# Optimization experiments

Hardware: AMD Instinct MI355X
Metric: run time of the kernel (lower is better)

## Reference

```python
import jax, jax.numpy as jnp
import numpy as np

B, T_ENC, T_DEC, D, N_STATE = 32, 1024, 512, 512, 512


def setup_inputs() -> dict:
    key = jax.random.key(0)
    k1, k2, k3, k4 = jax.random.split(key, 4)
    scale = 1.0 / np.sqrt(D)
    return {
        "states_encoder": jax.random.normal(k1, (B, T_ENC, D), dtype=jnp.float32),
        "states_decoder": jax.random.normal(k2, (B, T_DEC, N_STATE), dtype=jnp.float32),
        "Wk": jax.random.normal(k3, (D, N_STATE), dtype=jnp.float32) * scale,
        "bk": jnp.zeros((N_STATE,), dtype=jnp.float32),
        "Wv": jax.random.normal(k4, (D, N_STATE), dtype=jnp.float32) * scale,
        "bv": jnp.zeros((N_STATE,), dtype=jnp.float32),
    }


def reference(states_encoder, states_decoder, Wk, bk, Wv, bv):
    # general Luong dot-product attention (n_state = int branch)
    key_vector = states_encoder @ Wk + bk          # [B, T_enc, N]
    val_vector = states_encoder @ Wv + bv          # [B, T_enc, N]
    # score[b, t_dec, t_enc] = sum_n dec[b,t_dec,n] * key[b,t_enc,n]
    score = jnp.einsum('bqn,bkn->bqk', states_decoder, key_vector)
    attention = jax.nn.softmax(score, axis=-1)     # over encoder positions
    # context[b, t_dec, n] = sum_k attention[b,t_dec,k] * val[b,k,n]
    context = jnp.einsum('bqk,bkn->bqn', attention, val_vector)
    return (context, attention)
```

## Files before the change

### kernel.cpp

```cpp
#include <hip/hip_runtime.h>
#include <math.h>

#define BB    32
#define TENC  1024
#define TDEC  512
#define DDIM  512
#define NST   512

typedef _Float16 f16_t;
typedef _Float16 f16x8 __attribute__((ext_vector_type(8)));
typedef _Float16 f16x4 __attribute__((ext_vector_type(4)));
typedef float    f32x4 __attribute__((ext_vector_type(4)));

#define GLOAD_LDS16(gp, lp) __builtin_amdgcn_global_load_lds( \
    (const __attribute__((address_space(1))) unsigned int*)(const void*)(gp), \
    (__attribute__((address_space(3))) unsigned int*)(lp), 16, 0, 0)

static __device__ __forceinline__ f32x4 MFMA16H(f16x8 a, f16x8 b, f32x4 c) {
    return __builtin_amdgcn_mfma_f32_16x16x32_f16(a, b, c, 0, 0, 0);
}

__global__ __launch_bounds__(256)
void cvt_f32_f16(const float* __restrict__ x, f16_t* __restrict__ y, long n8)
{
    long i = (long)blockIdx.x * 256 + threadIdx.x;
    if (i >= n8) return;
    float4 a = *(const float4*)&x[i * 8];
    float4 b = *(const float4*)&x[i * 8 + 4];
    f16x8 o;
    o[0] = (f16_t)a.x; o[1] = (f16_t)a.y; o[2] = (f16_t)a.z; o[3] = (f16_t)a.w;
    o[4] = (f16_t)b.x; o[5] = (f16_t)b.y; o[6] = (f16_t)b.z; o[7] = (f16_t)b.w;
    *(f16x8*)&y[i * 8] = o;
}

__global__ __launch_bounds__(256)
void transpose_to_f16(const float* __restrict__ in, f16_t* __restrict__ out,
                      int R, int C)
{
    __shared__ f16_t tile[64][65];
    const int c0 = blockIdx.x * 64, r0 = blockIdx.y * 64;
    const int t = threadIdx.x;
    const int rr = t >> 4;
    const int cc = (t & 15) * 4;
#pragma unroll
    for (int p = 0; p < 4; ++p) {
        int r = rr + p * 16;
        float4 v = *(const float4*)&in[(long)(r0 + r) * C + c0 + cc];
        tile[r][cc + 0] = (f16_t)v.x;
        tile[r][cc + 1] = (f16_t)v.y;
        tile[r][cc + 2] = (f16_t)v.z;
        tile[r][cc + 3] = (f16_t)v.w;
    }
    __syncthreads();
    const int dr = t >> 2;
    const int tc = (t & 3) * 16;
    f16_t tmp[16];
#pragma unroll
    for (int e = 0; e < 16; ++e) tmp[e] = tile[tc + e][dr];
    *(f16x8*)&out[(long)(c0 + dr) * R + r0 + tc]     = *(f16x8*)&tmp[0];
    *(f16x8*)&out[(long)(c0 + dr) * R + r0 + tc + 8] = *(f16x8*)&tmp[8];
}

template<int EPI>
__global__ __launch_bounds__(256)
void gemm_h(const f16_t* __restrict__ A, const f16_t* __restrict__ B,
            const float* __restrict__ bias, void* __restrict__ C0,
            int M, int N, int K, long sA, long sB, long sC)
{
    __shared__ f16_t lds[2][8192];

    const int tid  = threadIdx.x;
    const int wave = tid >> 6;
    const int lane = tid & 63;

    const int gx = gridDim.x, gy = gridDim.y;
    const long nwg = (long)gx * gy * gridDim.z;
    const long fo  = ((long)blockIdx.z * gy + blockIdx.y) * gx + blockIdx.x;
    const long f2 = (fo & 7) * (nwg >> 3) + (fo >> 3);
    const int bx  = (int)(f2 % gx);
    const int by  = (int)((f2 / gx) % gy);
    const long bz = f2 / ((long)gx * gy);

    const f16_t* Ab = A + bz * sA;
    const f16_t* Bb = B + bz * sB;

    const int row0 = by * 128;
    const int col0 = bx * 128;

    const int srow  = wave * 16 + (lane >> 2);
    const int sslot = (lane & 3) ^ ((srow >> 1) & 3);
    const int wdst  = wave * 512;
    const long aOff0 = (long)(row0 + srow) * K + sslot * 8;
    const long aOff1 = (long)(row0 + 64 + srow) * K + sslot * 8;
    const long bOff0 = (long)(col0 + srow) * K + sslot * 8;
    const long bOff1 = (long)(col0 + 64 + srow) * K + sslot * 8;

    const int fr = lane & 15;
    const int q  = lane >> 4;
    const int wr = (wave >> 1) * 64;
    const int wc = (wave & 1) * 64;
    int aro[4], bro[4];
#pragma unroll
    for (int i = 0; i < 4; ++i) {
        const int r = wr + i * 16 + fr;
        aro[i] = r * 32 + ((q ^ ((r >> 1) & 3)) * 8);
    }
#pragma unroll
    for (int j = 0; j < 4; ++j) {
        const int r = wc + j * 16 + fr;
        bro[j] = r * 32 + ((q ^ ((r >> 1) & 3)) * 8);
    }

    f32x4 acc[4][4] = {};
    const int NT = K >> 5;

#define STAGE(buf, kt) do {                                   \
        GLOAD_LDS16(Ab + aOff0 + (kt), &(buf)[wdst]);         \
        GLOAD_LDS16(Ab + aOff1 + (kt), &(buf)[2048 + wdst]);  \
        GLOAD_LDS16(Bb + bOff0 + (kt), &(buf)[4096 + wdst]);  \
        GLOAD_LDS16(Bb + bOff1 + (kt), &(buf)[6144 + wdst]);  \
    } while (0)

    STAGE(lds[0], 0);

    for (int t = 0; t < NT; ++t) {
        const f16_t* cur = lds[t & 1];
        f16_t* nxt = lds[(t & 1) ^ 1];
        const bool pf = (t + 1 < NT);

        __builtin_amdgcn_sched_barrier(0);
        __builtin_amdgcn_s_barrier();
        if (pf) {
            STAGE(nxt, (t + 1) << 5);
            asm volatile("s_waitcnt vmcnt(4)" ::: "memory");
        } else {
            asm volatile("s_waitcnt vmcnt(0)" ::: "memory");
        }
        __builtin_amdgcn_s_barrier();
        __builtin_amdgcn_sched_barrier(0);

        f16x8 aH[4], bH[4];
#pragma unroll
        for (int i = 0; i < 4; ++i) aH[i] = *(const f16x8*)&cur[aro[i]];
#pragma unroll
        for (int j = 0; j < 4; ++j) bH[j] = *(const f16x8*)&cur[4096 + bro[j]];

#pragma unroll
        for (int j = 0; j < 4; ++j)
#pragma unroll
            for (int i = 0; i < 4; ++i)
                acc[i][j] = MFMA16H(aH[i], bH[j], acc[i][j]);
    }
#undef STAGE

    const int frow = q * 4;
#pragma unroll
    for (int i = 0; i < 4; ++i) {
        const int rgl = row0 + wr + i * 16 + frow;
#pragma unroll
        for (int j = 0; j < 4; ++j) {
            const int cg = col0 + wc + j * 16 + fr;
            if constexpr (EPI == 0) {
                float* C = (float*)C0 + bz * sC;
#pragma unroll
                for (int r = 0; r < 4; ++r)
                    C[(long)(rgl + r) * N + cg] = acc[i][j][r];
            } else if constexpr (EPI == 2) {
                f16_t* C = (f16_t*)C0 + bz * sC;
#pragma unroll
                for (int r = 0; r < 4; ++r)
                    C[(long)(rgl + r) * N + cg] = (f16_t)acc[i][j][r];
            } else {
                float* C = (float*)C0 + bz * sC;
                const float badd = bias[cg];
#pragma unroll
                for (int r = 0; r < 4; ++r)
                    C[(long)(rgl + r) * N + cg] = acc[i][j][r] + badd;
            }
        }
    }
}

__global__ __launch_bounds__(256)
void softmax_rows(float* __restrict__ S, f16_t* __restrict__ Sh)
{
    const long row = (long)blockIdx.x * 4 + (threadIdx.x >> 6);
    const int lane = threadIdx.x & 63;
    float* p = S + row * (long)TENC;

    float4 v[4];
    float m = -INFINITY;
#pragma unroll
    for (int i = 0; i < 4; ++i) {
        v[i] = *(const float4*)&p[i * 256 + lane * 4];
        m = fmaxf(fmaxf(fmaxf(v[i].x, v[i].y), fmaxf(v[i].z, v[i].w)), m);
    }
#pragma unroll
    for (int o = 32; o; o >>= 1) m = fmaxf(m, __shfl_xor(m, o, 64));

    float s = 0.f;
#pragma unroll
    for (int i = 0; i < 4; ++i) {
        v[i].x = __expf(v[i].x - m);
        v[i].y = __expf(v[i].y - m);
        v[i].z = __expf(v[i].z - m);
        v[i].w = __expf(v[i].w - m);
        s += v[i].x + v[i].y + v[i].z + v[i].w;
    }
#pragma unroll
    for (int o = 32; o; o >>= 1) s += __shfl_xor(s, o, 64);

    const float inv = 1.0f / s;
#pragma unroll
    for (int i = 0; i < 4; ++i) {
        v[i].x *= inv; v[i].y *= inv; v[i].z *= inv; v[i].w *= inv;
        *(float4*)&p[i * 256 + lane * 4] = v[i];
        if (Sh) {
            f16x4 h;
            h[0] = (f16_t)v[i].x; h[1] = (f16_t)v[i].y;
            h[2] = (f16_t)v[i].z; h[3] = (f16_t)v[i].w;
            *(f16x4*)&Sh[row * (long)TENC + i * 256 + lane * 4] = h;
        }
    }
}

#define TILE_M 64
#define TILE_N 64
#define TILE_K 16
template<bool B_TRANS, bool ADD_BIAS>
__global__ __launch_bounds__(256)
void gemm_f32(const float* __restrict__ A, const float* __restrict__ Bm,
              const float* __restrict__ bias, float* __restrict__ C,
              int M, int N, int K, int lda, int ldb,
              long strideA, long strideB, long strideC)
{
    __shared__ float As[TILE_K][TILE_M + 4];
    __shared__ float Bs[TILE_K][TILE_N + 4];
    const int b = blockIdx.z;
    A += (long)b * strideA; Bm += (long)b * strideB; C += (long)b * strideC;
    const int tid = threadIdx.x;
    const int tx = tid & 15, ty = tid >> 4;
    const int row0 = blockIdx.y * TILE_M, col0 = blockIdx.x * TILE_N;
    const int am = tid >> 2, ak = (tid & 3) * 4;
    float acc[4][4] = {};
    for (int kt = 0; kt < K; kt += TILE_K) {
        float4 a4 = *(const float4*)&A[(long)(row0 + am) * lda + kt + ak];
        float4 b4;
        if (B_TRANS) b4 = *(const float4*)&Bm[(long)(col0 + am) * ldb + kt + ak];
        else {
            const int bk_ = tid >> 4, bn = (tid & 15) * 4;
            b4 = *(const float4*)&Bm[(long)(kt + bk_) * ldb + col0 + bn];
        }
        __syncthreads();
        As[ak + 0][am] = a4.x; As[ak + 1][am] = a4.y;
        As[ak + 2][am] = a4.z; As[ak + 3][am] = a4.w;
        if (B_TRANS) {
            Bs[ak + 0][am] = b4.x; Bs[ak + 1][am] = b4.y;
            Bs[ak + 2][am] = b4.z; Bs[ak + 3][am] = b4.w;
        } else {
            const int bk_ = tid >> 4, bn = (tid & 15) * 4;
            *(float4*)&Bs[bk_][bn] = b4;
        }
        __syncthreads();
#pragma unroll
        for (int k = 0; k < TILE_K; ++k) {
            float4 av = *(const float4*)&As[k][ty * 4];
            float4 bv4 = *(const float4*)&Bs[k][tx * 4];
            float ar[4] = {av.x, av.y, av.z, av.w};
            float br[4] = {bv4.x, bv4.y, bv4.z, bv4.w};
#pragma unroll
            for (int i = 0; i < 4; ++i)
#pragma unroll
                for (int j = 0; j < 4; ++j)
                    acc[i][j] = fmaf(ar[i], br[j], acc[i][j]);
        }
    }
    float4 bias4 = make_float4(0.f, 0.f, 0.f, 0.f);
    if (ADD_BIAS) bias4 = *(const float4*)&bias[col0 + tx * 4];
#pragma unroll
    for (int i = 0; i < 4; ++i) {
        float4 o;
        o.x = acc[i][0] + bias4.x; o.y = acc[i][1] + bias4.y;
        o.z = acc[i][2] + bias4.z; o.w = acc[i][3] + bias4.w;
        *(float4*)&C[(long)(row0 + ty * 4 + i) * N + col0 + tx * 4] = o;
    }
}

extern "C" void kernel_launch(void* const* d_in, const int* in_sizes, int n_in,
                              void* d_out, int out_size, void* d_ws, size_t ws_size,
                              hipStream_t stream)
{
    const float* enc = (const float*)d_in[0];
    const float* dec = (const float*)d_in[1];
    const float* Wk  = (const float*)d_in[2];
    const float* Wv  = (const float*)d_in[4];
    const float* bv  = (const float*)d_in[5];

    const long nE = (long)BB * TENC * DDIM;
    const long nD = (long)BB * TDEC * NST;
    const long nW = (long)DDIM * NST;

    float* ctx   = (float*)d_out;
    float* attnF = ctx + nD;

    const size_t need = 68157440;
    const dim3 blk(256);

    if (ws_size < need) {
        float* ws = (float*)d_ws;
        gemm_f32<true, false><<<dim3(DDIM / 64, (BB * TDEC) / 64, 1), blk, 0, stream>>>(
            dec, Wk, nullptr, ws, BB * TDEC, DDIM, NST, NST, NST, 0, 0, 0);
        gemm_f32<true, false><<<dim3(TENC / 64, TDEC / 64, BB), blk, 0, stream>>>(
            ws, enc, nullptr, attnF, TDEC, TENC, DDIM, DDIM, DDIM,
            (long)TDEC * DDIM, (long)TENC * DDIM, (long)TDEC * TENC);
        softmax_rows<<<(BB * TDEC) / 4, blk, 0, stream>>>(attnF, nullptr);
        gemm_f32<false, false><<<dim3(DDIM / 64, TDEC / 64, BB), blk, 0, stream>>>(
            attnF, enc, nullptr, ws, TDEC, DDIM, TENC, TENC, DDIM,
            (long)TDEC * TENC, (long)TENC * DDIM, (long)TDEC * DDIM);
        gemm_f32<false, true><<<dim3(NST / 64, (BB * TDEC) / 64, 1), blk, 0, stream>>>(
            ws, Wv, bv, ctx, BB * TDEC, NST, DDIM, DDIM, NST, 0, 0, 0);
        return;
    }

    char* w = (char*)d_ws;
    f16_t* EVT   = (f16_t*)(w);
    f16_t* Ef16  = (f16_t*)(w + 33554432);
    f16_t* Wk16  = (f16_t*)(w + 67108864);
    f16_t* WvT16 = (f16_t*)(w + 67633152);
    f16_t* attnB = Ef16;

    f16_t* dec16 = (f16_t*)ctx;
    f16_t* DK16  = dec16 + nD;

    cvt_f32_f16<<<(unsigned)(nE / 8 / 256), blk, 0, stream>>>(enc, Ef16, nE / 8);
    cvt_f32_f16<<<(unsigned)(nD / 8 / 256), blk, 0, stream>>>(dec, dec16, nD / 8);
    cvt_f32_f16<<<(unsigned)(nW / 8 / 256), blk, 0, stream>>>(Wk, Wk16, nW / 8);
    transpose_to_f16<<<dim3(NST / 64, DDIM / 64, 1), blk, 0, stream>>>(Wv, WvT16, DDIM, NST);

    gemm_h<2><<<dim3(DDIM / 128, (BB * TDEC) / 128, 1), blk, 0, stream>>>(
        dec16, Wk16, nullptr, DK16,
        BB * TDEC, DDIM, NST, 0, 0, 0);

    gemm_h<0><<<dim3(TENC / 128, TDEC / 128, BB), blk, 0, stream>>>(
        DK16, Ef16, nullptr, attnF,
        TDEC, TENC, DDIM,
        (long)TDEC * DDIM, (long)TENC * DDIM, (long)TDEC * TENC);

    gemm_h<2><<<dim3(TENC / 128, NST / 128, BB), blk, 0, stream>>>(
        WvT16, Ef16, nullptr, EVT,
        NST, TENC, DDIM,
        0, (long)TENC * DDIM, (long)NST * TENC);

    softmax_rows<<<(BB * TDEC) / 4, blk, 0, stream>>>(attnF, attnB);

    gemm_h<3><<<dim3(NST / 128, TDEC / 128, BB), blk, 0, stream>>>(
        attnB, EVT, bv, ctx,
        TDEC, NST, TENC,
        (long)TDEC * TENC, (long)NST * TENC, (long)TDEC * NST);
}
```

Measured before the change: 157.5 us.

## Fuse score GEMM with softmax and read fp32 attention directly in context GEMM

```diff
diff --git a/kernel.cpp b/kernel.cpp
--- a/kernel.cpp
+++ b/kernel.cpp
@@ -21,31 +21,37 @@
 }
 
 __global__ __launch_bounds__(256)
-void cvt_f32_f16(const float* __restrict__ x, f16_t* __restrict__ y, long n8)
+void prep_convert(const float* __restrict__ enc, const float* __restrict__ dec,
+                  const float* __restrict__ Wk, const float* __restrict__ Wv,
+                  f16_t* __restrict__ Ef16, f16_t* __restrict__ dec16,
+                  f16_t* __restrict__ Wk16, f16_t* __restrict__ WvT16)
 {
-    long i = (long)blockIdx.x * 256 + threadIdx.x;
-    if (i >= n8) return;
-    float4 a = *(const float4*)&x[i * 8];
-    float4 b = *(const float4*)&x[i * 8 + 4];
-    f16x8 o;
-    o[0] = (f16_t)a.x; o[1] = (f16_t)a.y; o[2] = (f16_t)a.z; o[3] = (f16_t)a.w;
-    o[4] = (f16_t)b.x; o[5] = (f16_t)b.y; o[6] = (f16_t)b.z; o[7] = (f16_t)b.w;
-    *(f16x8*)&y[i * 8] = o;
-}
-
-__global__ __launch_bounds__(256)
-void transpose_to_f16(const float* __restrict__ in, f16_t* __restrict__ out,
-                      int R, int C)
-{
+    const int bid = blockIdx.x;
+    const int t = threadIdx.x;
+
+    if (bid < 12416) {
+        const float* src; f16_t* dst; long i;
+        if (bid < 8192)       { src = enc; dst = Ef16;  i = (long)bid * 256 + t; }
+        else if (bid < 12288) { src = dec; dst = dec16; i = (long)(bid - 8192) * 256 + t; }
+        else                  { src = Wk;  dst = Wk16;  i = (long)(bid - 12288) * 256 + t; }
+        float4 a = *(const float4*)&src[i * 8];
+        float4 b = *(const float4*)&src[i * 8 + 4];
+        f16x8 o;
+        o[0] = (f16_t)a.x; o[1] = (f16_t)a.y; o[2] = (f16_t)a.z; o[3] = (f16_t)a.w;
+        o[4] = (f16_t)b.x; o[5] = (f16_t)b.y; o[6] = (f16_t)b.z; o[7] = (f16_t)b.w;
+        *(f16x8*)&dst[i * 8] = o;
+        return;
+    }
+
     __shared__ f16_t tile[64][65];
-    const int c0 = blockIdx.x * 64, r0 = blockIdx.y * 64;
-    const int t = threadIdx.x;
+    const int r2 = bid - 12416;
+    const int c0 = (r2 & 7) * 64, r0 = (r2 >> 3) * 64;
     const int rr = t >> 4;
     const int cc = (t & 15) * 4;
 #pragma unroll
     for (int p = 0; p < 4; ++p) {
         int r = rr + p * 16;
-        float4 v = *(const float4*)&in[(long)(r0 + r) * C + c0 + cc];
+        float4 v = *(const float4*)&Wv[(long)(r0 + r) * NST + c0 + cc];
         tile[r][cc + 0] = (f16_t)v.x;
         tile[r][cc + 1] = (f16_t)v.y;
         tile[r][cc + 2] = (f16_t)v.z;
@@ -57,8 +63,8 @@
     f16_t tmp[16];
 #pragma unroll
     for (int e = 0; e < 16; ++e) tmp[e] = tile[tc + e][dr];
-    *(f16x8*)&out[(long)(c0 + dr) * R + r0 + tc]     = *(f16x8*)&tmp[0];
-    *(f16x8*)&out[(long)(c0 + dr) * R + r0 + tc + 8] = *(f16x8*)&tmp[8];
+    *(f16x8*)&WvT16[(long)(c0 + dr) * DDIM + r0 + tc]     = *(f16x8*)&tmp[0];
+    *(f16x8*)&WvT16[(long)(c0 + dr) * DDIM + r0 + tc + 8] = *(f16x8*)&tmp[8];
 }
 
 template<int EPI>
@@ -160,19 +166,14 @@
 #pragma unroll
         for (int j = 0; j < 4; ++j) {
             const int cg = col0 + wc + j * 16 + fr;
-            if constexpr (EPI == 0) {
-                float* C = (float*)C0 + bz * sC;
-#pragma unroll
-                for (int r = 0; r < 4; ++r)
-                    C[(long)(rgl + r) * N + cg] = acc[i][j][r];
-            } else if constexpr (EPI == 2) {
+            if constexpr (EPI == 2) {
                 f16_t* C = (f16_t*)C0 + bz * sC;
 #pragma unroll
                 for (int r = 0; r < 4; ++r)
                     C[(long)(rgl + r) * N + cg] = (f16_t)acc[i][j][r];
             } else {
                 float* C = (float*)C0 + bz * sC;
-                const float badd = bias[cg];
+                const float badd = (EPI == 3) ? bias[cg] : 0.0f;
 #pragma unroll
                 for (int r = 0; r < 4; ++r)
                     C[(long)(rgl + r) * N + cg] = acc[i][j][r] + badd;
@@ -181,13 +182,313 @@
     }
 }
 
+__global__ __launch_bounds__(512)
+void score_softmax(const f16_t* __restrict__ DK, const f16_t* __restrict__ E,
+                   float* __restrict__ attn)
+{
+    __shared__ f16_t Bs[1024 * 32];
+    __shared__ f16_t As[32 * 32];
+    __shared__ float smx[8][32];
+    __shared__ float sms[8][32];
+
+    const int tid  = threadIdx.x;
+    const int wave = tid >> 6;
+    const int lane = tid & 63;
+
+    const int fo = blockIdx.y * 16 + blockIdx.x;
+    const int f2 = (fo & 7) * 64 + (fo >> 3);
+    const int rg = f2 & 15;
+    const int z  = f2 >> 4;
+
+    const f16_t* DKb = DK + ((long)z * TDEC + rg * 32) * DDIM;
+    const f16_t* Eb  = E + (long)z * TENC * DDIM;
+    float* Ab = attn + (long)z * TDEC * TENC + (long)(rg * 32) * TENC;
+
+    const int srow = lane >> 2;
+    const int sk   = lane & 3;
+
+    const int fr = lane & 15;
+    const int q  = lane >> 4;
+    const int wc = wave * 128;
+    int aro[2], bro[8];
+#pragma unroll
+    for (int i = 0; i < 2; ++i) {
+        const int r = i * 16 + fr;
+        aro[i] = r * 32 + ((q ^ ((r >> 1) & 3)) * 8);
+    }
+#pragma unroll
+    for (int j = 0; j < 8; ++j) {
+        const int r = wc + j * 16 + fr;
+        bro[j] = r * 32 + ((q ^ ((r >> 1) & 3)) * 8);
+    }
+
+    f32x4 acc[2][8] = {};
+
+#define SSTAGE(ktd) do {                                                       \
+        _Pragma("unroll")                                                      \
+        for (int c = 0; c < 8; ++c) {                                          \
+            const int rL = wave * 128 + c * 16 + srow;                         \
+            const int slot = sk ^ ((rL >> 1) & 3);                             \
+            GLOAD_LDS16(Eb + (long)rL * DDIM + (ktd) + slot * 8,               \
+                        &Bs[(wave * 128 + c * 16) * 32]);                      \
+        }                                                                      \
+        if (wave == 0) {                                                       \
+            _Pragma("unroll")                                                  \
+            for (int c = 0; c < 2; ++c) {                                      \
+                const int rA = c * 16 + srow;                                  \
+                const int slot = sk ^ ((rA >> 1) & 3);                         \
+                GLOAD_LDS16(DKb + (long)rA * DDIM + (ktd) + slot * 8,          \
+                            &As[c * 16 * 32]);                                 \
+            }                                                                  \
+        }                                                                      \
+    } while (0)
+
+    SSTAGE(0);
+
+    for (int kt = 0; kt < 16; ++kt) {
+        asm volatile("s_waitcnt vmcnt(0)" ::: "memory");
+        __builtin_amdgcn_s_barrier();
+        __builtin_amdgcn_sched_barrier(0);
+
+        f16x8 aH[2];
+        aH[0] = *(const f16x8*)&As[aro[0]];
+        aH[1] = *(const f16x8*)&As[aro[1]];
+#pragma unroll
+        for (int j = 0; j < 8; ++j) {
+            f16x8 bH = *(const f16x8*)&Bs[bro[j]];
+            acc[0][j] = MFMA16H(aH[0], bH, acc[0][j]);
+            acc[1][j] = MFMA16H(aH[1], bH, acc[1][j]);
+        }
+        asm volatile("s_waitcnt lgkmcnt(0)" ::: "memory");
+        __builtin_amdgcn_sched_barrier(0);
+        __builtin_amdgcn_s_barrier();
+        if (kt < 15) SSTAGE((kt + 1) * 32);
+    }
+#undef SSTAGE
+
+    float pm[2][4];
+#pragma unroll
+    for (int i = 0; i < 2; ++i)
+#pragma unroll
+        for (int rr = 0; rr < 4; ++rr) {
+            float m = acc[i][0][rr];
+#pragma unroll
+            for (int j = 1; j < 8; ++j) m = fmaxf(m, acc[i][j][rr]);
+            pm[i][rr] = m;
+        }
+#pragma unroll
+    for (int o = 1; o < 16; o <<= 1)
+#pragma unroll
+        for (int i = 0; i < 2; ++i)
+#pragma unroll
+            for (int rr = 0; rr < 4; ++rr)
+                pm[i][rr] = fmaxf(pm[i][rr], __shfl_xor(pm[i][rr], o, 16));
+    if (fr == 0) {
+#pragma unroll
+        for (int i = 0; i < 2; ++i)
+#pragma unroll
+            for (int rr = 0; rr < 4; ++rr)
+                smx[wave][i * 16 + q * 4 + rr] = pm[i][rr];
+    }
+    __syncthreads();
+    float gm[2][4];
+#pragma unroll
+    for (int i = 0; i < 2; ++i)
+#pragma unroll
+        for (int rr = 0; rr < 4; ++rr) {
+            const int row = i * 16 + q * 4 + rr;
+            float m = smx[0][row];
+#pragma unroll
+            for (int w = 1; w < 8; ++w) m = fmaxf(m, smx[w][row]);
+            gm[i][rr] = m;
+        }
+    float ps[2][4] = {};
+#pragma unroll
+    for (int i = 0; i < 2; ++i)
+#pragma unroll
+        for (int j = 0; j < 8; ++j)
+#pragma unroll
+            for (int rr = 0; rr < 4; ++rr) {
+                float e = __expf(acc[i][j][rr] - gm[i][rr]);
+                acc[i][j][rr] = e;
+                ps[i][rr] += e;
+            }
+#pragma unroll
+    for (int o = 1; o < 16; o <<= 1)
+#pragma unroll
+        for (int i = 0; i < 2; ++i)
+#pragma unroll
+            for (int rr = 0; rr < 4; ++rr)
+                ps[i][rr] += __shfl_xor(ps[i][rr], o, 16);
+    if (fr == 0) {
+#pragma unroll
+        for (int i = 0; i < 2; ++i)
+#pragma unroll
+            for (int rr = 0; rr < 4; ++rr)
+                sms[wave][i * 16 + q * 4 + rr] = ps[i][rr];
+    }
+    __syncthreads();
+#pragma unroll
+    for (int i = 0; i < 2; ++i)
+#pragma unroll
+        for (int rr = 0; rr < 4; ++rr) {
+            const int row = i * 16 + q * 4 + rr;
+            float s = sms[0][row];
+#pragma unroll
+            for (int w = 1; w < 8; ++w) s += sms[w][row];
+            const float inv = 1.0f / s;
+#pragma unroll
+            for (int j = 0; j < 8; ++j)
+                Ab[(long)row * TENC + wc + j * 16 + fr] = acc[i][j][rr] * inv;
+        }
+}
+
 __global__ __launch_bounds__(256)
-void softmax_rows(float* __restrict__ S, f16_t* __restrict__ Sh)
+void gemm_ctx(const float* __restrict__ Af, const f16_t* __restrict__ Bh,
+              const float* __restrict__ bias, float* __restrict__ C,
+              int M, int N, int K, long sAf, long sB, long sC)
+{
+    __shared__ f16_t lds[2][8192];
+
+    const int tid  = threadIdx.x;
+    const int wave = tid >> 6;
+    const int lane = tid & 63;
+
+    const int gx = gridDim.x, gy = gridDim.y;
+    const long nwg = (long)gx * gy * gridDim.z;
+    const long fo  = ((long)blockIdx.z * gy + blockIdx.y) * gx + blockIdx.x;
+    const long f2 = (fo & 7) * (nwg >> 3) + (fo >> 3);
+    const int bx  = (int)(f2 % gx);
+    const int by  = (int)((f2 / gx) % gy);
+    const long bz = f2 / ((long)gx * gy);
+
+    const float* AfB = Af + bz * sAf;
+    const f16_t* BhB = Bh + bz * sB;
+
+    const int row0 = by * 128;
+    const int col0 = bx * 128;
+
+    const int srow  = wave * 16 + (lane >> 2);
+    const int sslot = (lane & 3) ^ ((srow >> 1) & 3);
+    const int wdst  = wave * 512;
+
+    const int rrow = tid >> 3;
+    const int rk4  = (tid & 7) * 4;
+    const int rgr  = rk4 >> 3;
+    const int rh4  = rk4 & 4;
+
+    const int fr = lane & 15;
+    const int q  = lane >> 4;
+    const int wr = (wave >> 1) * 64;
+    const int wc = (wave & 1) * 64;
+    int aro[4], bro[4];
+#pragma unroll
+    for (int i = 0; i < 4; ++i) {
+        const int r = wr + i * 16 + fr;
+        aro[i] = r * 32 + ((q ^ ((r >> 1) & 3)) * 8);
+    }
+#pragma unroll
+    for (int j = 0; j < 4; ++j) {
+        const int r = wc + j * 16 + fr;
+        bro[j] = r * 32 + ((q ^ ((r >> 1) & 3)) * 8);
+    }
+
+    f32x4 acc[4][4] = {};
+    float4 rS[4];
+    f16x8 aH[4], bH[4];
+    const int NT = K >> 5;
+
+    auto stageG = [&](f16_t* buf, int kt) {
+#pragma unroll
+        for (int c = 0; c < 2; ++c) {
+            const long go = (long)(col0 + c * 64 + srow) * K + kt + sslot * 8;
+            GLOAD_LDS16(BhB + go, &buf[4096 + c * 2048 + wdst]);
+        }
+    };
+    auto loadR = [&](int kt) {
+#pragma unroll
+        for (int i = 0; i < 4; ++i)
+            rS[i] = *(const float4*)&AfB[(long)(row0 + i * 32 + rrow) * K + kt + rk4];
+    };
+    auto writeR = [&](f16_t* buf) {
+#pragma unroll
+        for (int i = 0; i < 4; ++i) {
+            const int row = i * 32 + rrow;
+            const int eo  = row * 32 + ((rgr ^ ((row >> 1) & 3)) * 8) + rh4;
+            f16x4 h4;
+            h4[0] = (f16_t)rS[i].x; h4[1] = (f16_t)rS[i].y;
+            h4[2] = (f16_t)rS[i].z; h4[3] = (f16_t)rS[i].w;
+            *(f16x4*)&buf[eo] = h4;
+        }
+    };
+    auto readF = [&](const f16_t* buf) {
+#pragma unroll
+        for (int i = 0; i < 4; ++i) aH[i] = *(const f16x8*)&buf[aro[i]];
+#pragma unroll
+        for (int j = 0; j < 4; ++j) bH[j] = *(const f16x8*)&buf[4096 + bro[j]];
+    };
+
+    loadR(0);
+    stageG(lds[0], 0);
+    writeR(lds[0]);
+    loadR(32);
+    asm volatile("s_waitcnt vmcnt(4)" ::: "memory");
+    asm volatile("s_waitcnt lgkmcnt(0)" ::: "memory");
+    __builtin_amdgcn_s_barrier();
+    readF(lds[0]);
+    asm volatile("s_waitcnt lgkmcnt(0)" ::: "memory");
+    __builtin_amdgcn_s_barrier();
+
+    for (int t = 0; t < NT; ++t) {
+        f16_t* nxt = lds[(t & 1) ^ 1];
+        const bool pf = (t + 1 < NT);
+
+        if (pf) {
+            writeR(nxt);
+            stageG(nxt, (t + 1) << 5);
+            if (t + 2 < NT) loadR((t + 2) << 5);
+        }
+#pragma unroll
+        for (int j = 0; j < 4; ++j)
+#pragma unroll
+            for (int i = 0; i < 4; ++i)
+                acc[i][j] = MFMA16H(aH[i], bH[j], acc[i][j]);
+
+        if (pf && (t + 2 < NT))
+            asm volatile("s_waitcnt vmcnt(4)" ::: "memory");
+        else
+            asm volatile("s_waitcnt vmcnt(0)" ::: "memory");
+        asm volatile("s_waitcnt lgkmcnt(0)" ::: "memory");
+        __builtin_amdgcn_s_barrier();
+        if (pf) {
+            readF(nxt);
+            asm volatile("s_waitcnt lgkmcnt(0)" ::: "memory");
+        }
+        __builtin_amdgcn_s_barrier();
+    }
+
+    const int frow = q * 4;
+#pragma unroll
+    for (int i = 0; i < 4; ++i) {
+        const int rgl = row0 + wr + i * 16 + frow;
+#pragma unroll
+        for (int j = 0; j < 4; ++j) {
+            const int cg = col0 + wc + j * 16 + fr;
+            float* Cp = C + bz * sC;
+            const float badd = bias[cg];
+#pragma unroll
+            for (int r = 0; r < 4; ++r)
+                Cp[(long)(rgl + r) * N + cg] = acc[i][j][r] + badd;
+        }
+    }
+}
+
+__global__ __launch_bounds__(256)
+void softmax_rows(float* __restrict__ S)
 {
     const long row = (long)blockIdx.x * 4 + (threadIdx.x >> 6);
     const int lane = threadIdx.x & 63;
     float* p = S + row * (long)TENC;
-
     float4 v[4];
     float m = -INFINITY;
 #pragma unroll
@@ -197,30 +498,20 @@
     }
 #pragma unroll
     for (int o = 32; o; o >>= 1) m = fmaxf(m, __shfl_xor(m, o, 64));
-
     float s = 0.f;
 #pragma unroll
     for (int i = 0; i < 4; ++i) {
-        v[i].x = __expf(v[i].x - m);
-        v[i].y = __expf(v[i].y - m);
-        v[i].z = __expf(v[i].z - m);
-        v[i].w = __expf(v[i].w - m);
+        v[i].x = __expf(v[i].x - m); v[i].y = __expf(v[i].y - m);
+        v[i].z = __expf(v[i].z - m); v[i].w = __expf(v[i].w - m);
         s += v[i].x + v[i].y + v[i].z + v[i].w;
     }
 #pragma unroll
     for (int o = 32; o; o >>= 1) s += __shfl_xor(s, o, 64);
-
     const float inv = 1.0f / s;
 #pragma unroll
     for (int i = 0; i < 4; ++i) {
         v[i].x *= inv; v[i].y *= inv; v[i].z *= inv; v[i].w *= inv;
         *(float4*)&p[i * 256 + lane * 4] = v[i];
-        if (Sh) {
-            f16x4 h;
-            h[0] = (f16_t)v[i].x; h[1] = (f16_t)v[i].y;
-            h[2] = (f16_t)v[i].z; h[3] = (f16_t)v[i].w;
-            *(f16x4*)&Sh[row * (long)TENC + i * 256 + lane * 4] = h;
-        }
     }
 }
 
@@ -296,9 +587,7 @@
     const float* Wv  = (const float*)d_in[4];
     const float* bv  = (const float*)d_in[5];
 
-    const long nE = (long)BB * TENC * DDIM;
     const long nD = (long)BB * TDEC * NST;
-    const long nW = (long)DDIM * NST;
 
     float* ctx   = (float*)d_out;
     float* attnF = ctx + nD;
@@ -313,7 +602,7 @@
         gemm_f32<true, false><<<dim3(TENC / 64, TDEC / 64, BB), blk, 0, stream>>>(
             ws, enc, nullptr, attnF, TDEC, TENC, DDIM, DDIM, DDIM,
             (long)TDEC * DDIM, (long)TENC * DDIM, (long)TDEC * TENC);
-        softmax_rows<<<(BB * TDEC) / 4, blk, 0, stream>>>(attnF, nullptr);
+        softmax_rows<<<(BB * TDEC) / 4, blk, 0, stream>>>(attnF);
         gemm_f32<false, false><<<dim3(DDIM / 64, TDEC / 64, BB), blk, 0, stream>>>(
             attnF, enc, nullptr, ws, TDEC, DDIM, TENC, TENC, DDIM,
             (long)TDEC * TENC, (long)TENC * DDIM, (long)TDEC * DDIM);
@@ -327,34 +616,26 @@
     f16_t* Ef16  = (f16_t*)(w + 33554432);
     f16_t* Wk16  = (f16_t*)(w + 67108864);
     f16_t* WvT16 = (f16_t*)(w + 67633152);
-    f16_t* attnB = Ef16;
 
     f16_t* dec16 = (f16_t*)ctx;
     f16_t* DK16  = dec16 + nD;
 
-    cvt_f32_f16<<<(unsigned)(nE / 8 / 256), blk, 0, stream>>>(enc, Ef16, nE / 8);
-    cvt_f32_f16<<<(unsigned)(nD / 8 / 256), blk, 0, stream>>>(dec, dec16, nD / 8);
-    cvt_f32_f16<<<(unsigned)(nW / 8 / 256), blk, 0, stream>>>(Wk, Wk16, nW / 8);
-    transpose_to_f16<<<dim3(NST / 64, DDIM / 64, 1), blk, 0, stream>>>(Wv, WvT16, DDIM, NST);
+    prep_convert<<<12480, blk, 0, stream>>>(enc, dec, Wk, Wv,
+                                            Ef16, dec16, Wk16, WvT16);
 
     gemm_h<2><<<dim3(DDIM / 128, (BB * TDEC) / 128, 1), blk, 0, stream>>>(
         dec16, Wk16, nullptr, DK16,
         BB * TDEC, DDIM, NST, 0, 0, 0);
-
-    gemm_h<0><<<dim3(TENC / 128, TDEC / 128, BB), blk, 0, stream>>>(
-        DK16, Ef16, nullptr, attnF,
-        TDEC, TENC, DDIM,
-        (long)TDEC * DDIM, (long)TENC * DDIM, (long)TDEC * TENC);
 
     gemm_h<2><<<dim3(TENC / 128, NST / 128, BB), blk, 0, stream>>>(
         WvT16, Ef16, nullptr, EVT,
         NST, TENC, DDIM,
         0, (long)TENC * DDIM, (long)NST * TENC);
 
-    softmax_rows<<<(BB * TDEC) / 4, blk, 0, stream>>>(attnF, attnB);
-
-    gemm_h<3><<<dim3(NST / 128, TDEC / 128, BB), blk, 0, stream>>>(
-        attnB, EVT, bv, ctx,
+    score_softmax<<<dim3(16, 32), dim3(512), 0, stream>>>(DK16, Ef16, attnF);
+
+    gemm_ctx<<<dim3(NST / 128, TDEC / 128, BB), blk, 0, stream>>>(
+        attnF, EVT, bv, ctx,
         TDEC, NST, TENC,
         (long)TDEC * TENC, (long)NST * TENC, (long)TDEC * NST);
 }
```

Result: slower. 160.9 us (+2.2%).

## Fuse fp32-to-fp16 conversion into GEMM operand loads and drop separate convert passes

Applied to the files above, without the earlier changes.

```diff
diff --git a/kernel.cpp b/kernel.cpp
--- a/kernel.cpp
+++ b/kernel.cpp
@@ -21,31 +21,32 @@
 }
 
 __global__ __launch_bounds__(256)
-void cvt_f32_f16(const float* __restrict__ x, f16_t* __restrict__ y, long n8)
-{
-    long i = (long)blockIdx.x * 256 + threadIdx.x;
-    if (i >= n8) return;
-    float4 a = *(const float4*)&x[i * 8];
-    float4 b = *(const float4*)&x[i * 8 + 4];
-    f16x8 o;
-    o[0] = (f16_t)a.x; o[1] = (f16_t)a.y; o[2] = (f16_t)a.z; o[3] = (f16_t)a.w;
-    o[4] = (f16_t)b.x; o[5] = (f16_t)b.y; o[6] = (f16_t)b.z; o[7] = (f16_t)b.w;
-    *(f16x8*)&y[i * 8] = o;
-}
-
-__global__ __launch_bounds__(256)
-void transpose_to_f16(const float* __restrict__ in, f16_t* __restrict__ out,
-                      int R, int C)
-{
+void prep_weights(const float* __restrict__ Wk, const float* __restrict__ Wv,
+                  f16_t* __restrict__ Wk16, f16_t* __restrict__ WvT16)
+{
+    const int bid = blockIdx.x;
+    const int t = threadIdx.x;
+
+    if (bid < 128) {
+        long i = (long)bid * 256 + t;
+        float4 a = *(const float4*)&Wk[i * 8];
+        float4 b = *(const float4*)&Wk[i * 8 + 4];
+        f16x8 o;
+        o[0] = (f16_t)a.x; o[1] = (f16_t)a.y; o[2] = (f16_t)a.z; o[3] = (f16_t)a.w;
+        o[4] = (f16_t)b.x; o[5] = (f16_t)b.y; o[6] = (f16_t)b.z; o[7] = (f16_t)b.w;
+        *(f16x8*)&Wk16[i * 8] = o;
+        return;
+    }
+
     __shared__ f16_t tile[64][65];
-    const int c0 = blockIdx.x * 64, r0 = blockIdx.y * 64;
-    const int t = threadIdx.x;
+    const int r2 = bid - 128;
+    const int c0 = (r2 & 7) * 64, r0 = (r2 >> 3) * 64;
     const int rr = t >> 4;
     const int cc = (t & 15) * 4;
 #pragma unroll
     for (int p = 0; p < 4; ++p) {
         int r = rr + p * 16;
-        float4 v = *(const float4*)&in[(long)(r0 + r) * C + c0 + cc];
+        float4 v = *(const float4*)&Wv[(long)(r0 + r) * NST + c0 + cc];
         tile[r][cc + 0] = (f16_t)v.x;
         tile[r][cc + 1] = (f16_t)v.y;
         tile[r][cc + 2] = (f16_t)v.z;
@@ -57,15 +58,15 @@
     f16_t tmp[16];
 #pragma unroll
     for (int e = 0; e < 16; ++e) tmp[e] = tile[tc + e][dr];
-    *(f16x8*)&out[(long)(c0 + dr) * R + r0 + tc]     = *(f16x8*)&tmp[0];
-    *(f16x8*)&out[(long)(c0 + dr) * R + r0 + tc + 8] = *(f16x8*)&tmp[8];
-}
-
-template<int EPI>
+    *(f16x8*)&WvT16[(long)(c0 + dr) * DDIM + r0 + tc]     = *(f16x8*)&tmp[0];
+    *(f16x8*)&WvT16[(long)(c0 + dr) * DDIM + r0 + tc + 8] = *(f16x8*)&tmp[8];
+}
+
+template<int AREG, int EPI>
 __global__ __launch_bounds__(256)
-void gemm_h(const f16_t* __restrict__ A, const f16_t* __restrict__ B,
-            const float* __restrict__ bias, void* __restrict__ C0,
-            int M, int N, int K, long sA, long sB, long sC)
+void gemm_rs(const float* __restrict__ Rf, const f16_t* __restrict__ Gh,
+             const float* __restrict__ bias, void* __restrict__ C0,
+             int M, int N, int K, long sRf, long sG, long sC)
 {
     __shared__ f16_t lds[2][8192];
 
@@ -81,19 +82,24 @@
     const int by  = (int)((f2 / gx) % gy);
     const long bz = f2 / ((long)gx * gy);
 
-    const f16_t* Ab = A + bz * sA;
-    const f16_t* Bb = B + bz * sB;
+    const float* RfB = Rf + bz * sRf;
+    const f16_t* GhB = Gh + bz * sG;
 
     const int row0 = by * 128;
     const int col0 = bx * 128;
+    const int rbase = AREG ? row0 : col0;
+    const int gbase = AREG ? col0 : row0;
+    constexpr int rOff = AREG ? 0 : 4096;
+    constexpr int gOff = AREG ? 4096 : 0;
 
     const int srow  = wave * 16 + (lane >> 2);
     const int sslot = (lane & 3) ^ ((srow >> 1) & 3);
     const int wdst  = wave * 512;
-    const long aOff0 = (long)(row0 + srow) * K + sslot * 8;
-    const long aOff1 = (long)(row0 + 64 + srow) * K + sslot * 8;
-    const long bOff0 = (long)(col0 + srow) * K + sslot * 8;
-    const long bOff1 = (long)(col0 + 64 + srow) * K + sslot * 8;
+
+    const int rrow = tid >> 3;
+    const int rk4  = (tid & 7) * 4;
+    const int rgr  = rk4 >> 3;
+    const int rh4  = rk4 & 4;
 
     const int fr = lane & 15;
     const int q  = lane >> 4;
@@ -112,46 +118,78 @@
     }
 
     f32x4 acc[4][4] = {};
+    float4 rS[4];
+    f16x8 aH[4], bH[4];
     const int NT = K >> 5;
 
-#define STAGE(buf, kt) do {                                   \
-        GLOAD_LDS16(Ab + aOff0 + (kt), &(buf)[wdst]);         \
-        GLOAD_LDS16(Ab + aOff1 + (kt), &(buf)[2048 + wdst]);  \
-        GLOAD_LDS16(Bb + bOff0 + (kt), &(buf)[4096 + wdst]);  \
-        GLOAD_LDS16(Bb + bOff1 + (kt), &(buf)[6144 + wdst]);  \
-    } while (0)
-
-    STAGE(lds[0], 0);
+    auto stageG = [&](f16_t* buf, int kt) {
+#pragma unroll
+        for (int c = 0; c < 2; ++c) {
+            const long go = (long)(gbase + c * 64 + srow) * K + kt + sslot * 8;
+            GLOAD_LDS16(GhB + go, &buf[gOff + c * 2048 + wdst]);
+        }
+    };
+    auto loadR = [&](int kt) {
+#pragma unroll
+        for (int i = 0; i < 4; ++i)
+            rS[i] = *(const float4*)&RfB[(long)(rbase + i * 32 + rrow) * K + kt + rk4];
+    };
+    auto writeR = [&](f16_t* buf) {
+#pragma unroll
+        for (int i = 0; i < 4; ++i) {
+            const int row = i * 32 + rrow;
+            const int eo  = row * 32 + ((rgr ^ ((row >> 1) & 3)) * 8) + rh4;
+            f16x4 h4;
+            h4[0] = (f16_t)rS[i].x; h4[1] = (f16_t)rS[i].y;
+            h4[2] = (f16_t)rS[i].z; h4[3] = (f16_t)rS[i].w;
+            *(f16x4*)&buf[rOff + eo] = h4;
+        }
+    };
+    auto readF = [&](const f16_t* buf) {
+#pragma unroll
+        for (int i = 0; i < 4; ++i) aH[i] = *(const f16x8*)&buf[aro[i]];
+#pragma unroll
+        for (int j = 0; j < 4; ++j) bH[j] = *(const f16x8*)&buf[4096 + bro[j]];
+    };
+
+    loadR(0);
+    stageG(lds[0], 0);
+    writeR(lds[0]);
+    loadR(32);
+    asm volatile("s_waitcnt vmcnt(4)" ::: "memory");
+    asm volatile("s_waitcnt lgkmcnt(0)" ::: "memory");
+    __builtin_amdgcn_s_barrier();
+    readF(lds[0]);
+    asm volatile("s_waitcnt lgkmcnt(0)" ::: "memory");
+    __builtin_amdgcn_s_barrier();
 
     for (int t = 0; t < NT; ++t) {
-        const f16_t* cur = lds[t & 1];
         f16_t* nxt = lds[(t & 1) ^ 1];
         const bool pf = (t + 1 < NT);
 
-        __builtin_amdgcn_sched_barrier(0);
+        if (pf) {
+            writeR(nxt);
+            stageG(nxt, (t + 1) << 5);
+            if (t + 2 < NT) loadR((t + 2) << 5);
+        }
+#pragma unroll
+        for (int j = 0; j < 4; ++j)
+#pragma unroll
+            for (int i = 0; i < 4; ++i)
+                acc[i][j] = MFMA16H(aH[i], bH[j], acc[i][j]);
+
+        if (pf && (t + 2 < NT))
+            asm volatile("s_waitcnt vmcnt(4)" ::: "memory");
+        else
+            asm volatile("s_waitcnt vmcnt(0)" ::: "memory");
+        asm volatile("s_waitcnt lgkmcnt(0)" ::: "memory");
         __builtin_amdgcn_s_barrier();
         if (pf) {
-            STAGE(nxt, (t + 1) << 5);
-            asm volatile("s_waitcnt vmcnt(4)" ::: "memory");
-        } else {
-            asm volatile("s_waitcnt vmcnt(0)" ::: "memory");
+            readF(nxt);
+            asm volatile("s_waitcnt lgkmcnt(0)" ::: "memory");
         }
         __builtin_amdgcn_s_barrier();
-        __builtin_amdgcn_sched_barrier(0);
-
-        f16x8 aH[4], bH[4];
-#pragma unroll
-        for (int i = 0; i < 4; ++i) aH[i] = *(const f16x8*)&cur[aro[i]];
-#pragma unroll
-        for (int j = 0; j < 4; ++j) bH[j] = *(const f16x8*)&cur[4096 + bro[j]];
-
-#pragma unroll
-        for (int j = 0; j < 4; ++j)
-#pragma unroll
-            for (int i = 0; i < 4; ++i)
-                acc[i][j] = MFMA16H(aH[i], bH[j], acc[i][j]);
-    }
-#undef STAGE
+    }
 
     const int frow = q * 4;
 #pragma unroll
@@ -160,16 +198,16 @@
 #pragma unroll
         for (int j = 0; j < 4; ++j) {
             const int cg = col0 + wc + j * 16 + fr;
-            if constexpr (EPI == 0) {
+            if constexpr (EPI == 2) {
+                f16_t* C = (f16_t*)C0 + bz * sC;
+#pragma unroll
+                for (int r = 0; r < 4; ++r)
+                    C[(long)(rgl + r) * N + cg] = (f16_t)acc[i][j][r];
+            } else if constexpr (EPI == 0) {
                 float* C = (float*)C0 + bz * sC;
 #pragma unroll
                 for (int r = 0; r < 4; ++r)
                     C[(long)(rgl + r) * N + cg] = acc[i][j][r];
-            } else if constexpr (EPI == 2) {
-                f16_t* C = (f16_t*)C0 + bz * sC;
-#pragma unroll
-                for (int r = 0; r < 4; ++r)
-                    C[(long)(rgl + r) * N + cg] = (f16_t)acc[i][j][r];
             } else {
                 float* C = (float*)C0 + bz * sC;
                 const float badd = bias[cg];
@@ -182,7 +220,7 @@
 }
 
 __global__ __launch_bounds__(256)
-void softmax_rows(float* __restrict__ S, f16_t* __restrict__ Sh)
+void softmax_rows(float* __restrict__ S)
 {
     const long row = (long)blockIdx.x * 4 + (threadIdx.x >> 6);
     const int lane = threadIdx.x & 63;
@@ -215,12 +253,6 @@
     for (int i = 0; i < 4; ++i) {
         v[i].x *= inv; v[i].y *= inv; v[i].z *= inv; v[i].w *= inv;
         *(float4*)&p[i * 256 + lane * 4] = v[i];
-        if (Sh) {
-            f16x4 h;
-            h[0] = (f16_t)v[i].x; h[1] = (f16_t)v[i].y;
-            h[2] = (f16_t)v[i].z; h[3] = (f16_t)v[i].w;
-            *(f16x4*)&Sh[row * (long)TENC + i * 256 + lane * 4] = h;
-        }
     }
 }
 
@@ -296,14 +328,12 @@
     const float* Wv  = (const float*)d_in[4];
     const float* bv  = (const float*)d_in[5];
 
-    const long nE = (long)BB * TENC * DDIM;
     const long nD = (long)BB * TDEC * NST;
-    const long nW = (long)DDIM * NST;
 
     float* ctx   = (float*)d_out;
     float* attnF = ctx + nD;
 
-    const size_t need = 68157440;
+    const size_t need = 35127296;
     const dim3 blk(256);
 
     if (ws_size < need) {
@@ -313,7 +343,7 @@
         gemm_f32<true, false><<<dim3(TENC / 64, TDEC / 64, BB), blk, 0, stream>>>(
             ws, enc, nullptr, attnF, TDEC, TENC, DDIM, DDIM, DDIM,
             (long)TDEC * DDIM, (long)TENC * DDIM, (long)TDEC * TENC);
-        softmax_rows<<<(BB * TDEC) / 4, blk, 0, stream>>>(attnF, nullptr);
+        softmax_rows<<<(BB * TDEC) / 4, blk, 0, stream>>>(attnF);
         gemm_f32<false, false><<<dim3(DDIM / 64, TDEC / 64, BB), blk, 0, stream>>>(
             attnF, enc, nullptr, ws, TDEC, DDIM, TENC, TENC, DDIM,
             (long)TDEC * TENC, (long)TENC * DDIM, (long)TDEC * DDIM);
@@ -324,37 +354,31 @@
 
     char* w = (char*)d_ws;
     f16_t* EVT   = (f16_t*)(w);
-    f16_t* Ef16  = (f16_t*)(w + 33554432);
-    f16_t* Wk16  = (f16_t*)(w + 67108864);
-    f16_t* WvT16 = (f16_t*)(w + 67633152);
-    f16_t* attnB = Ef16;
-
-    f16_t* dec16 = (f16_t*)ctx;
-    f16_t* DK16  = dec16 + nD;
-
-    cvt_f32_f16<<<(unsigned)(nE / 8 / 256), blk, 0, stream>>>(enc, Ef16, nE / 8);
-    cvt_f32_f16<<<(unsigned)(nD / 8 / 256), blk, 0, stream>>>(dec, dec16, nD / 8);
-    cvt_f32_f16<<<(unsigned)(nW / 8 / 256), blk, 0, stream>>>(Wk, Wk16, nW / 8);
-    transpose_to_f16<<<dim3(NST / 64, DDIM / 64, 1), blk, 0, stream>>>(Wv, WvT16, DDIM, NST);
-
-    gemm_h<2><<<dim3(DDIM / 128, (BB * TDEC) / 128, 1), blk, 0, stream>>>(
-        dec16, Wk16, nullptr, DK16,
+    f16_t* Wk16  = (f16_t*)(w + 33554432);
+    f16_t* WvT16 = (f16_t*)(w + 34078720);
+
+    f16_t* DK16  = (f16_t*)ctx;
+
+    prep_weights<<<192, blk, 0, stream>>>(Wk, Wv, Wk16, WvT16);
+
+    gemm_rs<1, 2><<<dim3(DDIM / 128, (BB * TDEC) / 128, 1), blk, 0, stream>>>(
+        dec, Wk16, nullptr, DK16,
         BB * TDEC, DDIM, NST, 0, 0, 0);
 
-    gemm_h<0><<<dim3(TENC / 128, TDEC / 128, BB), blk, 0, stream>>>(
-        DK16, Ef16, nullptr, attnF,
+    gemm_rs<0, 2><<<dim3(TENC / 128, NST / 128, BB), blk, 0, stream>>>(
+        enc, WvT16, nullptr, EVT,
+        NST, TENC, DDIM,
+        (long)TENC * DDIM, 0, (long)NST * TENC);
+
+    gemm_rs<0, 0><<<dim3(TENC / 128, TDEC / 128, BB), blk, 0, stream>>>(
+        enc, DK16, nullptr, attnF,
         TDEC, TENC, DDIM,
-        (long)TDEC * DDIM, (long)TENC * DDIM, (long)TDEC * TENC);
-
-    gemm_h<2><<<dim3(TENC / 128, NST / 128, BB), blk, 0, stream>>>(
-        WvT16, Ef16, nullptr, EVT,
-        NST, TENC, DDIM,
-        0, (long)TENC * DDIM, (long)NST * TENC);
-
-    softmax_rows<<<(BB * TDEC) / 4, blk, 0, stream>>>(attnF, attnB);
-
-    gemm_h<3><<<dim3(NST / 128, TDEC / 128, BB), blk, 0, stream>>>(
-        attnB, EVT, bv, ctx,
+        (long)TENC * DDIM, (long)TDEC * DDIM, (long)TDEC * TENC);
+
+    softmax_rows<<<(BB * TDEC) / 4, blk, 0, stream>>>(attnF);
+
+    gemm_rs<1, 3><<<dim3(NST / 128, TDEC / 128, BB), blk, 0, stream>>>(
+        attnF, EVT, bv, ctx,
         TDEC, NST, TENC,
         (long)TDEC * TENC, (long)NST * TENC, (long)TDEC * NST);
 }
```

New measurement: 161.2 us. 1.02x slower.
